# Optimization experiments

Hardware: AMD Instinct MI355X
Metric: run time of the kernel (lower is better)

Reference implementation:

```python
import jax, jax.numpy as jnp
import numpy as np

N = 50000
E = 600000
NFEAT = 128
NHID = 128
PAD_N = 60000


def setup_inputs() -> dict:
    key = jax.random.key(0)
    ks = jax.random.split(key, 10)
    x = jax.random.normal(ks[0], (N, NFEAT), dtype=jnp.float32)
    edge_index = jax.random.randint(ks[1], (2, E), 0, N, dtype=jnp.int64)
    pos_idx = jnp.arange(N, dtype=jnp.int64)
    # SAGEConv params: lin_l (applied to mean-aggregated neighbors, with bias),
    # lin_r (applied to root/self features, no bias). Two layers.
    s1 = 1.0 / np.sqrt(NFEAT)
    s2 = 1.0 / np.sqrt(NHID)
    Wl1 = jax.random.uniform(ks[2], (NFEAT, NHID), jnp.float32, -s1, s1)
    Wr1 = jax.random.uniform(ks[3], (NFEAT, NHID), jnp.float32, -s1, s1)
    b1 = jax.random.uniform(ks[4], (NHID,), jnp.float32, -s1, s1)
    Wl2 = jax.random.uniform(ks[5], (NHID, NHID), jnp.float32, -s2, s2)
    Wr2 = jax.random.uniform(ks[6], (NHID, NHID), jnp.float32, -s2, s2)
    b2 = jax.random.uniform(ks[7], (NHID,), jnp.float32, -s2, s2)
    return {"x": x, "edge_index": edge_index, "pos_idx": pos_idx, "pad_n": PAD_N,
            "Wl1": Wl1, "Wr1": Wr1, "b1": b1, "Wl2": Wl2, "Wr2": Wr2, "b2": b2}


def _sage_conv(h, src, dst, Wl, Wr, b):
    # mean aggregation of source features into destination nodes
    msg = h[src]                                              # [E, F]
    agg = jax.ops.segment_sum(msg, dst, num_segments=N)       # [N, F]
    cnt = jax.ops.segment_sum(jnp.ones((dst.shape[0],), h.dtype), dst, num_segments=N)
    agg = agg / jnp.maximum(cnt, 1.0)[:, None]
    return agg @ Wl + h @ Wr + b


def reference(x, edge_index, pos_idx, pad_n, Wl1, Wr1, b1, Wl2, Wr2, b2):
    src, dst = edge_index[0], edge_index[1]
    h = jax.nn.relu(_sage_conv(x, src, dst, Wl1, Wr1, b1))
    # dropout is a no-op in eval mode (training=False)
    h = jax.nn.relu(_sage_conv(h, src, dst, Wl2, Wr2, b2))
    out = jnp.zeros((pad_n, h.shape[1]), h.dtype).at[pos_idx].set(h)
    return out
```

## Files before the change

kernel.cpp:

```cpp
#include <hip/hip_runtime.h>


#define NF 128
#define CAP 48

typedef _Float16 f16x8 __attribute__((ext_vector_type(8)));
typedef _Float16 f16x4 __attribute__((ext_vector_type(4)));
typedef float f32x4 __attribute__((ext_vector_type(4)));
typedef unsigned short u16;

__device__ __forceinline__ void swizzle_w(const float* __restrict__ Wl,
                                          const float* __restrict__ Wr,
                                          _Float16* __restrict__ Wf, int t) {
    int lane = t & 63;
    int frag = t >> 6;
    int s = frag >> 3, c = frag & 7;
    int n = s * 16 + (lane & 15);
    int kbase = c * 32 + (lane >> 4) * 8;
    f16x8 v;
#pragma unroll
    for (int j = 0; j < 8; ++j) {
        int k = kbase + j;
        float f = (k < NF) ? Wl[k * NF + n] : Wr[(k - NF) * NF + n];
        v[j] = (_Float16)f;
    }
    ((f16x8*)Wf)[frag * 64 + lane] = v;
}

__global__ void init_kernel(int4* __restrict__ deg4, int ndeg4,
                            const float* __restrict__ Wl1, const float* __restrict__ Wr1,
                            _Float16* __restrict__ Wf1,
                            const float* __restrict__ Wl2, const float* __restrict__ Wr2,
                            _Float16* __restrict__ Wf2) {
    int nbd = (ndeg4 + 255) >> 8;
    int b = blockIdx.x;
    if (b < nbd) {
        int i = b * 256 + threadIdx.x;
        if (i < ndeg4) deg4[i] = make_int4(0, 0, 0, 0);
    } else if (b < nbd + 16) {
        swizzle_w(Wl1, Wr1, Wf1, (b - nbd) * 256 + threadIdx.x);
    } else {
        swizzle_w(Wl2, Wr2, Wf2, (b - nbd - 16) * 256 + threadIdx.x);
    }
}

__global__ void front_kernel(const int* __restrict__ src, const int* __restrict__ dst,
                             int* __restrict__ deg, u16* __restrict__ csr, int E,
                             const float4* __restrict__ x4, f16x4* __restrict__ xh4, int n4x,
                             float4* __restrict__ tail, int n4tail) {
    int nbf = (E / 4 + 255) >> 8;
    int nbc = (n4x + 255) >> 8;
    int b = blockIdx.x;
    if (b < nbf) {
        int e0 = (b * 256 + threadIdx.x) * 4;
        if (e0 + 4 <= E) {
            int4 d4 = *(const int4*)(dst + e0);
            int4 s4 = *(const int4*)(src + e0);
            int sl0 = atomicAdd(&deg[d4.x], 1);
            int sl1 = atomicAdd(&deg[d4.y], 1);
            int sl2 = atomicAdd(&deg[d4.z], 1);
            int sl3 = atomicAdd(&deg[d4.w], 1);
            if (sl0 < CAP) csr[(size_t)d4.x * CAP + sl0] = (u16)s4.x;
            if (sl1 < CAP) csr[(size_t)d4.y * CAP + sl1] = (u16)s4.y;
            if (sl2 < CAP) csr[(size_t)d4.z * CAP + sl2] = (u16)s4.z;
            if (sl3 < CAP) csr[(size_t)d4.w * CAP + sl3] = (u16)s4.w;
        } else {
            for (int e = e0; e < E; ++e) {
                int d = dst[e];
                int slot = atomicAdd(&deg[d], 1);
                if (slot < CAP) csr[(size_t)d * CAP + slot] = (u16)src[e];
            }
        }
    } else if (b < nbf + nbc) {
        int i = (b - nbf) * 256 + threadIdx.x;
        if (i < n4x) {
            float4 v = x4[i];
            f16x4 o;
            o[0] = (_Float16)v.x; o[1] = (_Float16)v.y;
            o[2] = (_Float16)v.z; o[3] = (_Float16)v.w;
            xh4[i] = o;
        }
    } else {
        int i = (b - nbf - nbc) * 256 + threadIdx.x;
        if (i < n4tail) tail[i] = make_float4(0.f, 0.f, 0.f, 0.f);
    }
}

#define LDA 136
template <bool LAST>
__global__ __launch_bounds__(256) void sage_layer_fused(
    const u16* __restrict__ csr, const int* __restrict__ deg,
    const _Float16* __restrict__ H,
    const _Float16* __restrict__ Wf,
    const float* __restrict__ bias,
    const int* __restrict__ pos,
    _Float16* __restrict__ outh,
    float* __restrict__ outf,
    int Nn) {
    __shared__ _Float16 sA[16][LDA];

    const int wave = threadIdx.x >> 6;
    const int lane = threadIdx.x & 63;
    const int sub  = lane >> 4;
    const int li   = lane & 15;
    const int m0 = blockIdx.x * 16;

    {
        int n = m0 + wave * 4 + sub;
        float a[8] = {0.f, 0.f, 0.f, 0.f, 0.f, 0.f, 0.f, 0.f};
        float b[8] = {0.f, 0.f, 0.f, 0.f, 0.f, 0.f, 0.f, 0.f};
        float inv = 1.0f;
        if (n < Nn) {
            int dg = deg[n];
            int rs = n * CAP;
            int re = rs + ((dg < CAP) ? dg : CAP);
            const f16x8* Hp = (const f16x8*)H;
            int k = rs;
            for (; k + 4 <= re; k += 4) {
                ushort4 c4 = *(const ushort4*)(csr + k);
                f16x8 v0 = Hp[(size_t)c4.x * 16 + li];
                f16x8 v1 = Hp[(size_t)c4.y * 16 + li];
                f16x8 v2 = Hp[(size_t)c4.z * 16 + li];
                f16x8 v3 = Hp[(size_t)c4.w * 16 + li];
#pragma unroll
                for (int j = 0; j < 8; ++j) {
                    a[j] += (float)v0[j] + (float)v2[j];
                    b[j] += (float)v1[j] + (float)v3[j];
                }
            }
            if (k + 2 <= re) {
                f16x8 v0 = Hp[(size_t)csr[k] * 16 + li];
                f16x8 v1 = Hp[(size_t)csr[k + 1] * 16 + li];
#pragma unroll
                for (int j = 0; j < 8; ++j) { a[j] += (float)v0[j]; b[j] += (float)v1[j]; }
                k += 2;
            }
            if (k < re) {
                f16x8 v0 = Hp[(size_t)csr[k] * 16 + li];
#pragma unroll
                for (int j = 0; j < 8; ++j) a[j] += (float)v0[j];
            }
            inv = 1.0f / fmaxf((float)dg, 1.0f);
        }
        f16x8 r;
#pragma unroll
        for (int j = 0; j < 8; ++j) r[j] = (_Float16)((a[j] + b[j]) * inv);
        *(f16x8*)&sA[wave * 4 + sub][li * 8] = r;
    }

    f16x8 bfrag[2][8];
    const f16x8* wfp = (const f16x8*)Wf;
#pragma unroll
    for (int s = 0; s < 2; ++s)
#pragma unroll
        for (int c = 0; c < 8; ++c)
            bfrag[s][c] = wfp[((2 * wave + s) * 8 + c) * 64 + lane];

    __syncthreads();

    f32x4 acc[2] = {(f32x4){0.f, 0.f, 0.f, 0.f}, (f32x4){0.f, 0.f, 0.f, 0.f}};

#pragma unroll
    for (int c = 0; c < 4; ++c) {
        f16x8 af = *(const f16x8*)&sA[li][c * 32 + sub * 8];
        acc[0] = __builtin_amdgcn_mfma_f32_16x16x32_f16(af, bfrag[0][c], acc[0], 0, 0, 0);
        acc[1] = __builtin_amdgcn_mfma_f32_16x16x32_f16(af, bfrag[1][c], acc[1], 0, 0, 0);
    }
    {
        int nd = m0 + li; if (nd >= Nn) nd = Nn - 1;
        const _Float16* xrow = H + (size_t)nd * NF;
#pragma unroll
        for (int c = 0; c < 4; ++c) {
            f16x8 af = *(const f16x8*)(xrow + c * 32 + sub * 8);
            acc[0] = __builtin_amdgcn_mfma_f32_16x16x32_f16(af, bfrag[0][4 + c], acc[0], 0, 0, 0);
            acc[1] = __builtin_amdgcn_mfma_f32_16x16x32_f16(af, bfrag[1][4 + c], acc[1], 0, 0, 0);
        }
    }

#pragma unroll
    for (int s = 0; s < 2; ++s) {
        int feat = (2 * wave + s) * 16 + li;
        float bv = bias[feat];
#pragma unroll
        for (int r = 0; r < 4; ++r) {
            int node = m0 + sub * 4 + r;
            if (node < Nn) {
                float v = fmaxf(acc[s][r] + bv, 0.f);
                if (LAST) outf[(size_t)pos[node] * NF + feat] = v;
                else      outh[(size_t)node * NF + feat] = (_Float16)v;
            }
        }
    }
}

extern "C" void kernel_launch(void* const* d_in, const int* in_sizes, int n_in,
                              void* d_out, int out_size, void* d_ws, size_t ws_size,
                              hipStream_t stream) {
    const float* x   = (const float*)d_in[0];
    const int*   ei  = (const int*)d_in[1];
    const int*   pos = (const int*)d_in[2];
    const float* Wl1 = (const float*)d_in[4];
    const float* Wr1 = (const float*)d_in[5];
    const float* b1  = (const float*)d_in[6];
    const float* Wl2 = (const float*)d_in[7];
    const float* Wr2 = (const float*)d_in[8];
    const float* b2  = (const float*)d_in[9];
    float* out = (float*)d_out;

    const int Nn = in_sizes[0] / NF;
    const int E  = in_sizes[1] / 2;
    const int* src = ei;
    const int* dst = ei + E;
    const int pad_rows = out_size / NF;

    const int degN = (Nn + 3) & ~3;
    _Float16* xh   = (_Float16*)d_ws;
    _Float16* h1h  = xh + (size_t)Nn * NF;
    _Float16* Wf1  = h1h + (size_t)Nn * NF;
    _Float16* Wf2  = Wf1 + 64 * 64 * 8;
    int* deg       = (int*)(Wf2 + 64 * 64 * 8);
    u16* csr       = (u16*)(deg + degN);

    const int ZB = 256;

    int ndeg4 = degN / 4;
    int nbd = (ndeg4 + ZB - 1) / ZB;
    init_kernel<<<nbd + 32, ZB, 0, stream>>>((int4*)deg, ndeg4,
                                             Wl1, Wr1, Wf1, Wl2, Wr2, Wf2);

    int n4x = Nn * NF / 4;
    int n4tail = (pad_rows - Nn) * NF / 4;
    int nbf = (E / 4 + ZB - 1) / ZB;
    int nbc = (n4x + ZB - 1) / ZB;
    int nbt = (n4tail + ZB - 1) / ZB;
    front_kernel<<<nbf + nbc + nbt, ZB, 0, stream>>>(
        src, dst, deg, csr, E,
        (const float4*)x, (f16x4*)xh, n4x,
        (float4*)(out + (size_t)Nn * NF), n4tail);

    const int fblocks = (Nn + 15) / 16;
    sage_layer_fused<false><<<fblocks, ZB, 0, stream>>>(
        csr, deg, xh, Wf1, b1, nullptr, h1h, nullptr, Nn);
    sage_layer_fused<true><<<fblocks, ZB, 0, stream>>>(
        csr, deg, h1h, Wf2, b2, pos, nullptr, out, Nn);
}
```

Baseline: 206.8 us.

## Split each node's neighbor gather across two lanes groups with unrolled loads

Each block now handles 8 nodes instead of 16, with two 16-lane groups sharing one node and each taking alternate neighbor slots. The first 24 slots are gathered with a fully unrolled, predicated load batch to raise memory-level parallelism. The MFMA rows then hold partial sums, which are added pairwise in the epilogue, and odd rows get zero self features. This doubles the grid and the MFMA/weight-fragment load work per node, in exchange for shorter per-lane dependency chains on the irregular gather.

```diff
diff --git a/kernel.cpp b/kernel.cpp
--- a/kernel.cpp
+++ b/kernel.cpp
@@ -103,49 +103,55 @@
     const int lane = threadIdx.x & 63;
     const int sub  = lane >> 4;
     const int li   = lane & 15;
-    const int m0 = blockIdx.x * 16;
+    const int m0 = blockIdx.x * 8;
 
     {
-        int n = m0 + wave * 4 + sub;
+        const int q = wave * 4 + sub;
+        const int n = m0 + (q >> 1);
+        const int p = q & 1;
         float a[8] = {0.f, 0.f, 0.f, 0.f, 0.f, 0.f, 0.f, 0.f};
         float b[8] = {0.f, 0.f, 0.f, 0.f, 0.f, 0.f, 0.f, 0.f};
         float inv = 1.0f;
         if (n < Nn) {
             int dg = deg[n];
-            int rs = n * CAP;
-            int re = rs + ((dg < CAP) ? dg : CAP);
+            int dgc = (dg < CAP) ? dg : CAP;
+            const ushort4* cp = (const ushort4*)(csr + n * CAP);
+            ushort4 c0 = cp[0], c1 = cp[1], c2 = cp[2],
+                    c3 = cp[3], c4 = cp[4], c5 = cp[5];
+            u16 e[12];
+            e[0]  = p ? c0.y : c0.x;  e[1]  = p ? c0.w : c0.z;
+            e[2]  = p ? c1.y : c1.x;  e[3]  = p ? c1.w : c1.z;
+            e[4]  = p ? c2.y : c2.x;  e[5]  = p ? c2.w : c2.z;
+            e[6]  = p ? c3.y : c3.x;  e[7]  = p ? c3.w : c3.z;
+            e[8]  = p ? c4.y : c4.x;  e[9]  = p ? c4.w : c4.z;
+            e[10] = p ? c5.y : c5.x;  e[11] = p ? c5.w : c5.z;
             const f16x8* Hp = (const f16x8*)H;
-            int k = rs;
-            for (; k + 4 <= re; k += 4) {
-                ushort4 c4 = *(const ushort4*)(csr + k);
-                f16x8 v0 = Hp[(size_t)c4.x * 16 + li];
-                f16x8 v1 = Hp[(size_t)c4.y * 16 + li];
-                f16x8 v2 = Hp[(size_t)c4.z * 16 + li];
-                f16x8 v3 = Hp[(size_t)c4.w * 16 + li];
+            f16x8 z = {};
+            f16x8 v[12];
+#pragma unroll
+            for (int i = 0; i < 12; ++i) {
+                int slot = p + 2 * i;
+                v[i] = (slot < dgc) ? Hp[(size_t)e[i] * 16 + li] : z;
+            }
+#pragma unroll
+            for (int i = 0; i < 12; i += 2) {
 #pragma unroll
                 for (int j = 0; j < 8; ++j) {
-                    a[j] += (float)v0[j] + (float)v2[j];
-                    b[j] += (float)v1[j] + (float)v3[j];
+                    a[j] += (float)v[i][j];
+                    b[j] += (float)v[i + 1][j];
                 }
             }
-            if (k + 2 <= re) {
-                f16x8 v0 = Hp[(size_t)csr[k] * 16 + li];
-                f16x8 v1 = Hp[(size_t)csr[k + 1] * 16 + li];
-#pragma unroll
-                for (int j = 0; j < 8; ++j) { a[j] += (float)v0[j]; b[j] += (float)v1[j]; }
-                k += 2;
-            }
-            if (k < re) {
-                f16x8 v0 = Hp[(size_t)csr[k] * 16 + li];
-#pragma unroll
-                for (int j = 0; j < 8; ++j) a[j] += (float)v0[j];
+            for (int slot = p + 24; slot < dgc; slot += 2) {
+                f16x8 vv = Hp[(size_t)csr[n * CAP + slot] * 16 + li];
+#pragma unroll
+                for (int j = 0; j < 8; ++j) a[j] += (float)vv[j];
             }
             inv = 1.0f / fmaxf((float)dg, 1.0f);
         }
         f16x8 r;
 #pragma unroll
         for (int j = 0; j < 8; ++j) r[j] = (_Float16)((a[j] + b[j]) * inv);
-        *(f16x8*)&sA[wave * 4 + sub][li * 8] = r;
+        *(f16x8*)&sA[q][li * 8] = r;
     }
 
     f16x8 bfrag[2][8];
@@ -167,11 +173,13 @@
         acc[1] = __builtin_amdgcn_mfma_f32_16x16x32_f16(af, bfrag[1][c], acc[1], 0, 0, 0);
     }
     {
-        int nd = m0 + li; if (nd >= Nn) nd = Nn - 1;
+        int nd = m0 + (li >> 1); if (nd >= Nn) nd = Nn - 1;
+        const bool odd = (li & 1);
         const _Float16* xrow = H + (size_t)nd * NF;
+        f16x8 z = {};
 #pragma unroll
         for (int c = 0; c < 4; ++c) {
-            f16x8 af = *(const f16x8*)(xrow + c * 32 + sub * 8);
+            f16x8 af = odd ? z : *(const f16x8*)(xrow + c * 32 + sub * 8);
             acc[0] = __builtin_amdgcn_mfma_f32_16x16x32_f16(af, bfrag[0][4 + c], acc[0], 0, 0, 0);
             acc[1] = __builtin_amdgcn_mfma_f32_16x16x32_f16(af, bfrag[1][4 + c], acc[1], 0, 0, 0);
         }
@@ -182,10 +190,10 @@
         int feat = (2 * wave + s) * 16 + li;
         float bv = bias[feat];
 #pragma unroll
-        for (int r = 0; r < 4; ++r) {
-            int node = m0 + sub * 4 + r;
+        for (int j = 0; j < 2; ++j) {
+            int node = m0 + sub * 2 + j;
             if (node < Nn) {
-                float v = fmaxf(acc[s][r] + bv, 0.f);
+                float v = fmaxf(acc[s][2 * j] + acc[s][2 * j + 1] + bv, 0.f);
                 if (LAST) outf[(size_t)pos[node] * NF + feat] = v;
                 else      outh[(size_t)node * NF + feat] = (_Float16)v;
             }
@@ -238,7 +246,7 @@
         (const float4*)x, (f16x4*)xh, n4x,
         (float4*)(out + (size_t)Nn * NF), n4tail);
 
-    const int fblocks = (Nn + 15) / 16;
+    const int fblocks = (Nn + 7) / 8;
     sage_layer_fused<false><<<fblocks, ZB, 0, stream>>>(
         csr, deg, xh, Wf1, b1, nullptr, h1h, nullptr, Nn);
     sage_layer_fused<true><<<fblocks, ZB, 0, stream>>>(
```

Result: slower. 215.2 us (+4.1%).

## Split per-node degree counters into two halves and merge init into front kernel

Applied to the files above, without the earlier changes.

Each destination node now has two degree counters, one per edge parity, and each counter fills its own half of the fixed-capacity neighbor list. This halves contention on atomics for the same address during CSR construction. The aggregation reads both counters and walks both segments. The separate init kernel is replaced by a memset, and the weight swizzle is folded into the front kernel, removing one launch. The risk is that a node with more than 24 edges of one parity silently drops neighbors, where the old cap was 48 in total.

```diff
diff --git a/kernel.cpp b/kernel.cpp
--- a/kernel.cpp
+++ b/kernel.cpp
@@ -3,6 +3,7 @@
 
 #define NF 128
 #define CAP 48
+#define SEG 24
 
 typedef _Float16 f16x8 __attribute__((ext_vector_type(8)));
 typedef _Float16 f16x4 __attribute__((ext_vector_type(4)));
@@ -27,25 +28,12 @@
     ((f16x8*)Wf)[frag * 64 + lane] = v;
 }
 
-__global__ void init_kernel(int4* __restrict__ deg4, int ndeg4,
-                            const float* __restrict__ Wl1, const float* __restrict__ Wr1,
-                            _Float16* __restrict__ Wf1,
-                            const float* __restrict__ Wl2, const float* __restrict__ Wr2,
-                            _Float16* __restrict__ Wf2) {
-    int nbd = (ndeg4 + 255) >> 8;
-    int b = blockIdx.x;
-    if (b < nbd) {
-        int i = b * 256 + threadIdx.x;
-        if (i < ndeg4) deg4[i] = make_int4(0, 0, 0, 0);
-    } else if (b < nbd + 16) {
-        swizzle_w(Wl1, Wr1, Wf1, (b - nbd) * 256 + threadIdx.x);
-    } else {
-        swizzle_w(Wl2, Wr2, Wf2, (b - nbd - 16) * 256 + threadIdx.x);
-    }
-}
-
 __global__ void front_kernel(const int* __restrict__ src, const int* __restrict__ dst,
                              int* __restrict__ deg, u16* __restrict__ csr, int E,
+                             const float* __restrict__ Wl1, const float* __restrict__ Wr1,
+                             _Float16* __restrict__ Wf1,
+                             const float* __restrict__ Wl2, const float* __restrict__ Wr2,
+                             _Float16* __restrict__ Wf2,
                              const float4* __restrict__ x4, f16x4* __restrict__ xh4, int n4x,
                              float4* __restrict__ tail, int n4tail) {
     int nbf = (E / 4 + 255) >> 8;
@@ -56,23 +44,28 @@
         if (e0 + 4 <= E) {
             int4 d4 = *(const int4*)(dst + e0);
             int4 s4 = *(const int4*)(src + e0);
-            int sl0 = atomicAdd(&deg[d4.x], 1);
-            int sl1 = atomicAdd(&deg[d4.y], 1);
-            int sl2 = atomicAdd(&deg[d4.z], 1);
-            int sl3 = atomicAdd(&deg[d4.w], 1);
-            if (sl0 < CAP) csr[(size_t)d4.x * CAP + sl0] = (u16)s4.x;
-            if (sl1 < CAP) csr[(size_t)d4.y * CAP + sl1] = (u16)s4.y;
-            if (sl2 < CAP) csr[(size_t)d4.z * CAP + sl2] = (u16)s4.z;
-            if (sl3 < CAP) csr[(size_t)d4.w * CAP + sl3] = (u16)s4.w;
+            int sl0 = atomicAdd(&deg[2 * d4.x + 0], 1);
+            int sl1 = atomicAdd(&deg[2 * d4.y + 1], 1);
+            int sl2 = atomicAdd(&deg[2 * d4.z + 0], 1);
+            int sl3 = atomicAdd(&deg[2 * d4.w + 1], 1);
+            if (sl0 < SEG) csr[(size_t)d4.x * CAP + sl0] = (u16)s4.x;
+            if (sl1 < SEG) csr[(size_t)d4.y * CAP + SEG + sl1] = (u16)s4.y;
+            if (sl2 < SEG) csr[(size_t)d4.z * CAP + sl2] = (u16)s4.z;
+            if (sl3 < SEG) csr[(size_t)d4.w * CAP + SEG + sl3] = (u16)s4.w;
         } else {
             for (int e = e0; e < E; ++e) {
                 int d = dst[e];
-                int slot = atomicAdd(&deg[d], 1);
-                if (slot < CAP) csr[(size_t)d * CAP + slot] = (u16)src[e];
+                int p = e & 1;
+                int slot = atomicAdd(&deg[2 * d + p], 1);
+                if (slot < SEG) csr[(size_t)d * CAP + p * SEG + slot] = (u16)src[e];
             }
         }
-    } else if (b < nbf + nbc) {
-        int i = (b - nbf) * 256 + threadIdx.x;
+    } else if (b < nbf + 16) {
+        swizzle_w(Wl1, Wr1, Wf1, (b - nbf) * 256 + threadIdx.x);
+    } else if (b < nbf + 32) {
+        swizzle_w(Wl2, Wr2, Wf2, (b - nbf - 16) * 256 + threadIdx.x);
+    } else if (b < nbf + 32 + nbc) {
+        int i = (b - nbf - 32) * 256 + threadIdx.x;
         if (i < n4x) {
             float4 v = x4[i];
             f16x4 o;
@@ -81,7 +74,7 @@
             xh4[i] = o;
         }
     } else {
-        int i = (b - nbf - nbc) * 256 + threadIdx.x;
+        int i = (b - nbf - 32 - nbc) * 256 + threadIdx.x;
         if (i < n4tail) tail[i] = make_float4(0.f, 0.f, 0.f, 0.f);
     }
 }
@@ -111,36 +104,41 @@
         float b[8] = {0.f, 0.f, 0.f, 0.f, 0.f, 0.f, 0.f, 0.f};
         float inv = 1.0f;
         if (n < Nn) {
-            int dg = deg[n];
-            int rs = n * CAP;
-            int re = rs + ((dg < CAP) ? dg : CAP);
+            int2 dgp = *(const int2*)&deg[2 * n];
+            int dgT = dgp.x + dgp.y;
             const f16x8* Hp = (const f16x8*)H;
-            int k = rs;
-            for (; k + 4 <= re; k += 4) {
-                ushort4 c4 = *(const ushort4*)(csr + k);
-                f16x8 v0 = Hp[(size_t)c4.x * 16 + li];
-                f16x8 v1 = Hp[(size_t)c4.y * 16 + li];
-                f16x8 v2 = Hp[(size_t)c4.z * 16 + li];
-                f16x8 v3 = Hp[(size_t)c4.w * 16 + li];
-#pragma unroll
-                for (int j = 0; j < 8; ++j) {
-                    a[j] += (float)v0[j] + (float)v2[j];
-                    b[j] += (float)v1[j] + (float)v3[j];
+#pragma unroll
+            for (int seg = 0; seg < 2; ++seg) {
+                int dseg = seg ? dgp.y : dgp.x;
+                if (dseg > SEG) dseg = SEG;
+                int k = n * CAP + seg * SEG;
+                int re = k + dseg;
+                for (; k + 4 <= re; k += 4) {
+                    ushort4 c4 = *(const ushort4*)(csr + k);
+                    f16x8 v0 = Hp[(size_t)c4.x * 16 + li];
+                    f16x8 v1 = Hp[(size_t)c4.y * 16 + li];
+                    f16x8 v2 = Hp[(size_t)c4.z * 16 + li];
+                    f16x8 v3 = Hp[(size_t)c4.w * 16 + li];
+#pragma unroll
+                    for (int j = 0; j < 8; ++j) {
+                        a[j] += (float)v0[j] + (float)v2[j];
+                        b[j] += (float)v1[j] + (float)v3[j];
+                    }
+                }
+                if (k + 2 <= re) {
+                    f16x8 v0 = Hp[(size_t)csr[k] * 16 + li];
+                    f16x8 v1 = Hp[(size_t)csr[k + 1] * 16 + li];
+#pragma unroll
+                    for (int j = 0; j < 8; ++j) { a[j] += (float)v0[j]; b[j] += (float)v1[j]; }
+                    k += 2;
+                }
+                if (k < re) {
+                    f16x8 v0 = Hp[(size_t)csr[k] * 16 + li];
+#pragma unroll
+                    for (int j = 0; j < 8; ++j) a[j] += (float)v0[j];
                 }
             }
-            if (k + 2 <= re) {
-                f16x8 v0 = Hp[(size_t)csr[k] * 16 + li];
-                f16x8 v1 = Hp[(size_t)csr[k + 1] * 16 + li];
-#pragma unroll
-                for (int j = 0; j < 8; ++j) { a[j] += (float)v0[j]; b[j] += (float)v1[j]; }
-                k += 2;
-            }
-            if (k < re) {
-                f16x8 v0 = Hp[(size_t)csr[k] * 16 + li];
-#pragma unroll
-                for (int j = 0; j < 8; ++j) a[j] += (float)v0[j];
-            }
-            inv = 1.0f / fmaxf((float)dg, 1.0f);
+            inv = 1.0f / fmaxf((float)dgT, 1.0f);
         }
         f16x8 r;
 #pragma unroll
@@ -213,7 +211,7 @@
     const int* dst = ei + E;
     const int pad_rows = out_size / NF;
 
-    const int degN = (Nn + 3) & ~3;
+    const int degN = (2 * Nn + 3) & ~3;
     _Float16* xh   = (_Float16*)d_ws;
     _Float16* h1h  = xh + (size_t)Nn * NF;
     _Float16* Wf1  = h1h + (size_t)Nn * NF;
@@ -223,18 +221,16 @@
 
     const int ZB = 256;
 
-    int ndeg4 = degN / 4;
-    int nbd = (ndeg4 + ZB - 1) / ZB;
-    init_kernel<<<nbd + 32, ZB, 0, stream>>>((int4*)deg, ndeg4,
-                                             Wl1, Wr1, Wf1, Wl2, Wr2, Wf2);
+    hipMemsetAsync(deg, 0, (size_t)degN * sizeof(int), stream);
 
     int n4x = Nn * NF / 4;
     int n4tail = (pad_rows - Nn) * NF / 4;
     int nbf = (E / 4 + ZB - 1) / ZB;
     int nbc = (n4x + ZB - 1) / ZB;
     int nbt = (n4tail + ZB - 1) / ZB;
-    front_kernel<<<nbf + nbc + nbt, ZB, 0, stream>>>(
+    front_kernel<<<nbf + 32 + nbc + nbt, ZB, 0, stream>>>(
         src, dst, deg, csr, E,
+        Wl1, Wr1, Wf1, Wl2, Wr2, Wf2,
         (const float4*)x, (f16x4*)xh, n4x,
         (float4*)(out + (size_t)Nn * NF), n4tail);
 
```

After: 208.6 us. Within noise of the previous version (+0.9%).
